# Kernel optimization log

Measured on AMD Instinct MI355X. Metric: run time of the kernel, lower is better.

The kernel has to match this reference:

```python
import jax, jax.numpy as jnp
import numpy as np

B, S, H, NH, NL = 8, 768, 768, 12, 5
HD = H // NH


def setup_inputs() -> dict:
    key = jax.random.key(0)
    ks = jax.random.split(key, 14)
    lim = 1.0 / np.sqrt(H)
    u = lambda k, shape: jax.random.uniform(k, shape, jnp.float32, -lim, lim)
    inp = {}
    inp["hidden_states"] = jax.random.normal(ks[0], (B, S, H), jnp.float32)
    inp["language_ids"] = jax.random.randint(ks[1], (B,), 0, NL)
    inp["attention_mask"] = jnp.ones((B, S), jnp.int32)
    # per-language query/key Linear weights (torch Linear: y = x @ W.T + b)
    inp["Wq_lang"] = u(ks[2], (NL, H, H))
    inp["bq_lang"] = u(ks[3], (NL, H))
    inp["Wk_lang"] = u(ks[4], (NL, H, H))
    inp["bk_lang"] = u(ks[5], (NL, H))
    # nn.MultiheadAttention params
    inp["in_proj_w"] = u(ks[6], (3 * H, H))
    inp["in_proj_b"] = u(ks[7], (3 * H,))
    inp["out_proj_w"] = u(ks[8], (H, H))
    inp["out_proj_b"] = u(ks[9], (H,))
    # alignment matrices: initialized as eye in torch; perturb so products are non-trivial
    inp["align"] = jnp.eye(H, dtype=jnp.float32) + 0.02 * jax.random.normal(ks[10], (NL, NL, H, H), jnp.float32)
    # output projection + layer norm
    inp["proj_w"] = u(ks[11], (H, H))
    inp["proj_b"] = u(ks[12], (H,))
    inp["ln_g"] = jnp.ones((H,), jnp.float32)
    inp["ln_b"] = jnp.zeros((H,), jnp.float32)
    return inp


def reference(hidden_states, language_ids, attention_mask, Wq_lang, bq_lang, Wk_lang, bk_lang,
              in_proj_w, in_proj_b, out_proj_w, out_proj_b, align, proj_w, proj_b, ln_g, ln_b):
    b, s, h = hidden_states.shape
    lang = language_ids
    # language-routed query/key transforms (grouped GEMM via gather of per-lang weights)
    q = jnp.einsum('bsi,boi->bso', hidden_states, Wq_lang[lang]) + bq_lang[lang][:, None, :]
    k = jnp.einsum('bsi,boi->bso', hidden_states, Wk_lang[lang]) + bk_lang[lang][:, None, :]
    # nn.MultiheadAttention (eval mode, no dropout). Note: the torch module's
    # key_padding_mask is always all-False due to a masked_fill(-inf).bool() bug,
    # so no masking is applied -- reproduced faithfully here.
    wq, wk, wv = jnp.split(in_proj_w, 3, axis=0)
    bq_, bk_, bv_ = jnp.split(in_proj_b, 3)
    Q = (jnp.einsum('bsi,oi->bso', q, wq) + bq_).reshape(b, s, NH, HD)
    K = (jnp.einsum('bsi,oi->bso', k, wk) + bk_).reshape(b, s, NH, HD)
    V = (jnp.einsum('bsi,oi->bso', hidden_states, wv) + bv_).reshape(b, s, NH, HD)
    scores = jnp.einsum('bqhd,bkhd->bhqk', Q, K) / np.sqrt(HD).astype(np.float32)
    attn = jax.nn.softmax(scores, axis=-1)  # [b, nh, s, s]
    ctx = jnp.einsum('bhqk,bkhd->bqhd', attn, V).reshape(b, s, h)
    aligned = jnp.einsum('bsi,oi->bso', ctx, out_proj_w) + out_proj_b
    # pairwise alignment chain: for each i, aligned_i @ prod_{j: lang_j != lang_i} A[lang_i, lang_j]
    # (i==j skipped; same-language pairs skipped since no A exists)
    same = lang[:, None] == lang[None, :]  # [b, b]; diagonal is True -> identity
    sel = align[lang[:, None], lang[None, :]]  # [b, b, h, h]
    I = jnp.eye(h, dtype=hidden_states.dtype)
    Smat = jnp.where(same[:, :, None, None], I, sel)  # [b(i), b(j), h, h]
    def step(carry, Sj):  # carry [b,h,h], Sj [b,h,h] for one j across all i
        return carry @ Sj, None
    M, _ = jax.lax.scan(step, jnp.tile(I, (b, 1, 1)), jnp.swapaxes(Smat, 0, 1))
    aligned = jnp.einsum('bsh,bhk->bsk', aligned, M)
    # output projection + residual layer norm
    out = jnp.einsum('bsi,oi->bso', aligned, proj_w) + proj_b
    x = out + hidden_states
    mu = x.mean(-1, keepdims=True)
    var = x.var(-1, keepdims=True)
    return (x - mu) / jnp.sqrt(var + 1e-5) * ln_g + ln_b
```

## Files before the change

kernel.cpp:

```cpp
#include <hip/hip_runtime.h>

#define Bn 8
#define Sn 768
#define Hn 768
#define NHn 12
#define HDn 64
#define NLn 5

typedef unsigned short u16;
typedef __bf16 bf16x8 __attribute__((ext_vector_type(8)));
typedef short s16x8 __attribute__((ext_vector_type(8)));
typedef float f32x4 __attribute__((ext_vector_type(4)));
typedef unsigned short u16x4 __attribute__((ext_vector_type(4)));

static __device__ __forceinline__ float bf2f(u16 v) {
    return __uint_as_float(((unsigned)v) << 16);
}
static __device__ __forceinline__ u16 f2bf(float f) {
    unsigned u = __float_as_uint(f);
    unsigned r = u + 0x7fffu + ((u >> 16) & 1u);
    return (u16)(r >> 16);
}
static __device__ __forceinline__ bf16x8 ld8(const u16* p) {
    return *reinterpret_cast<const bf16x8*>(p);
}
static __device__ __forceinline__ void glds16(const u16* g, u16* l) {
    __builtin_amdgcn_global_load_lds(
        (const __attribute__((address_space(1))) void*)g,
        (__attribute__((address_space(3))) void*)l, 16, 0, 0);
}

#define PREP_NF2B 6912
#define PREP_NTR  1584
__global__ __launch_bounds__(256) void k_prep(
    const float* __restrict__ hidden, u16* __restrict__ hb,
    const float* __restrict__ ipw, u16* __restrict__ ipwb,
    const float* __restrict__ projw, u16* __restrict__ pjwb,
    const float* __restrict__ Wq, const float* __restrict__ Wk,
    const float* __restrict__ opw, u16* __restrict__ S, u16* __restrict__ opwT,
    const float* __restrict__ ipb,
    const float* __restrict__ bq_lang, const float* __restrict__ bk_lang,
    float* __restrict__ beff)
{
    __shared__ float T[64][65];
    const size_t HH = (size_t)Hn * Hn;
    const int bid = blockIdx.x, tid = threadIdx.x;
    if (bid < PREP_NF2B) {
        const int n0 = (int)(Bn * Sn * Hn / 4), n1 = (int)(3 * HH / 4), n2 = (int)(HH / 4);
        int i = bid * 256 + tid;
        const float* s; u16* d; int off;
        if (i < n0)                { s = hidden; d = hb;   off = i; }
        else if (i < n0 + n1)      { s = ipw;    d = ipwb; off = i - n0; }
        else if (i < n0 + n1 + n2) { s = projw;  d = pjwb; off = i - n0 - n1; }
        else return;
        float4 v = reinterpret_cast<const float4*>(s)[off];
        u16x4 o;
        o[0] = f2bf(v.x); o[1] = f2bf(v.y); o[2] = f2bf(v.z); o[3] = f2bf(v.w);
        reinterpret_cast<u16x4*>(d)[off] = o;
    } else if (bid < PREP_NF2B + PREP_NTR) {
        int b2 = bid - PREP_NF2B;
        int z = b2 / 144, r = b2 % 144;
        int bx = r % 12, by = r / 12;
        const float* src;
        u16* dst;
        if (z < 5)       { src = Wq + (size_t)z * HH;       dst = S + (size_t)z * HH; }
        else if (z < 10) { src = Wk + (size_t)(z - 5) * HH; dst = S + (size_t)z * HH; }
        else             { src = opw;                        dst = opwT; }
        int i0 = bx * 64, o0 = by * 64;
        int x = tid & 63, ys = tid >> 6;
        for (int rr = ys; rr < 64; rr += 4)
            T[rr][x] = src[(size_t)(o0 + rr) * Hn + i0 + x];
        __syncthreads();
        for (int rr = ys; rr < 64; rr += 4)
            dst[(size_t)(i0 + rr) * Hn + o0 + x] = f2bf(T[x][rr]);
    } else {
        int b3 = bid - PREP_NF2B - PREP_NTR;
        int ox = b3 % 3, y = b3 / 3;
        int o = ox * 256 + tid;
        int which = y / 5, l = y % 5;
        const float4* w = reinterpret_cast<const float4*>(ipw + (size_t)which * HH + (size_t)o * Hn);
        const float4* bv = reinterpret_cast<const float4*>(((which ? bk_lang : bq_lang) + (size_t)l * Hn));
        float s = 0.f;
        for (int j = 0; j < Hn / 4; ++j) {
            float4 a = w[j], b = bv[j];
            s += a.x * b.x + a.y * b.y + a.z * b.z + a.w * b.w;
        }
        s += ipb[which * Hn + o];
        beff[(size_t)(which * 5 + l) * Hn + o] = s;
    }
}

__global__ __launch_bounds__(256) void k_f2b1(
    const float* __restrict__ s, u16* __restrict__ d, int n)
{
    int i = blockIdx.x * 256 + threadIdx.x;
    if (i >= n) return;
    float4 v = reinterpret_cast<const float4*>(s)[i];
    u16x4 o;
    o[0] = f2bf(v.x); o[1] = f2bf(v.y); o[2] = f2bf(v.z); o[3] = f2bf(v.w);
    reinterpret_cast<u16x4*>(d)[i] = o;
}

__device__ __forceinline__ void gemm128(
    const u16* __restrict__ A, int lda,
    const u16* __restrict__ Bw, int ldb,
    const float* __restrict__ bias,
    const float* __restrict__ addres,
    u16* __restrict__ outH, float* __restrict__ outF,
    u16* __restrict__ outVT, int ldc,
    int K, int m0, int n0, float scale)
{
    __shared__ u16 As[2][128 * 32];
    __shared__ u16 Bs[2][128 * 32];
    const int tid = threadIdx.x;
    const int lane = tid & 63, wave = tid >> 6;
    const int lrow = lane & 15, lquad = lane >> 4;
    const int wm = (wave >> 1) * 64, wn = (wave & 1) * 64;

    const int s0 = tid, s1 = tid + 256;
    const u16* gA0 = A + (size_t)(m0 + (s0 >> 2)) * lda + (s0 & 3) * 8;
    const u16* gA1 = A + (size_t)(m0 + (s1 >> 2)) * lda + (s1 & 3) * 8;
    const u16* gB0 = Bw + (size_t)(n0 + (s0 >> 2)) * ldb + (s0 & 3) * 8;
    const u16* gB1 = Bw + (size_t)(n0 + (s1 >> 2)) * ldb + (s1 & 3) * 8;

    f32x4 z = {0.f, 0.f, 0.f, 0.f};
    f32x4 acc[4][4];
    #pragma unroll
    for (int i = 0; i < 4; ++i)
        #pragma unroll
        for (int j = 0; j < 4; ++j) acc[i][j] = z;

    const int NT = K >> 5;
    auto stage = [&](int buf, int k0) {
        glds16(gA0 + k0, &As[buf][s0 * 8]);
        glds16(gA1 + k0, &As[buf][s1 * 8]);
        glds16(gB0 + k0, &Bs[buf][s0 * 8]);
        glds16(gB1 + k0, &Bs[buf][s1 * 8]);
    };
    auto compute = [&](int buf) {
        bf16x8 af[4], bf_[4];
        #pragma unroll
        for (int i = 0; i < 4; ++i)
            af[i] = ld8(&As[buf][(wm + i * 16 + lrow) * 32 + lquad * 8]);
        #pragma unroll
        for (int j = 0; j < 4; ++j)
            bf_[j] = ld8(&Bs[buf][(wn + j * 16 + lrow) * 32 + lquad * 8]);
        #pragma unroll
        for (int i = 0; i < 4; ++i)
            #pragma unroll
            for (int j = 0; j < 4; ++j)
                acc[i][j] = __builtin_amdgcn_mfma_f32_16x16x32_bf16(af[i], bf_[j], acc[i][j], 0, 0, 0);
    };

    stage(0, 0);
    __syncthreads();
    for (int kt = 1; kt < NT; ++kt) {
        stage(kt & 1, kt * 32);
        compute((kt - 1) & 1);
        __syncthreads();
    }
    compute((NT - 1) & 1);

    #pragma unroll
    for (int i = 0; i < 4; ++i) {
        #pragma unroll
        for (int j = 0; j < 4; ++j) {
            int col = n0 + wn + j * 16 + lrow;
            float bv = bias ? bias[col] : 0.f;
            if (outVT) {
                int row0 = m0 + wm + i * 16 + lquad * 4;
                int bb = row0 / Sn, s = row0 % Sn;
                int hh = col >> 6, dd = col & 63;
                u16x4 o;
                #pragma unroll
                for (int r = 0; r < 4; ++r) o[r] = f2bf((acc[i][j][r] + bv) * scale);
                *reinterpret_cast<u16x4*>(
                    outVT + (((size_t)bb * NHn + hh) * 64 + dd) * Sn + s) = o;
            } else {
                #pragma unroll
                for (int r = 0; r < 4; ++r) {
                    int row = m0 + wm + i * 16 + lquad * 4 + r;
                    float v = (acc[i][j][r] + bv) * scale;
                    if (addres) v += addres[(size_t)row * ldc + col];
                    if (outF) outF[(size_t)row * ldc + col] = v;
                    else      outH[(size_t)row * ldc + col] = f2bf(v);
                }
            }
        }
    }
}

__device__ __forceinline__ void gemm64(
    const u16* __restrict__ A, const u16* __restrict__ Bw,
    u16* __restrict__ outH, int K, int m0, int n0)
{
    __shared__ u16 As[2][64 * 32];
    __shared__ u16 Bs[2][64 * 32];
    const int tid = threadIdx.x;
    const int lane = tid & 63, wave = tid >> 6;
    const int lrow = lane & 15, lquad = lane >> 4;
    const int wm = (wave >> 1) * 32, wn = (wave & 1) * 32;

    const int row = tid >> 2, seg = tid & 3;
    const u16* gA = A + (size_t)(m0 + row) * Hn + seg * 8;
    const u16* gB = Bw + (size_t)(n0 + row) * Hn + seg * 8;

    f32x4 z = {0.f, 0.f, 0.f, 0.f};
    f32x4 acc[2][2];
    #pragma unroll
    for (int i = 0; i < 2; ++i)
        #pragma unroll
        for (int j = 0; j < 2; ++j) acc[i][j] = z;

    const int NT = K >> 5;
    auto stage = [&](int buf, int k0) {
        glds16(gA + k0, &As[buf][tid * 8]);
        glds16(gB + k0, &Bs[buf][tid * 8]);
    };
    auto compute = [&](int buf) {
        bf16x8 af[2], bf_[2];
        #pragma unroll
        for (int i = 0; i < 2; ++i)
            af[i] = ld8(&As[buf][(wm + i * 16 + lrow) * 32 + lquad * 8]);
        #pragma unroll
        for (int j = 0; j < 2; ++j)
            bf_[j] = ld8(&Bs[buf][(wn + j * 16 + lrow) * 32 + lquad * 8]);
        #pragma unroll
        for (int i = 0; i < 2; ++i)
            #pragma unroll
            for (int j = 0; j < 2; ++j)
                acc[i][j] = __builtin_amdgcn_mfma_f32_16x16x32_bf16(af[i], bf_[j], acc[i][j], 0, 0, 0);
    };

    stage(0, 0);
    __syncthreads();
    for (int kt = 1; kt < NT; ++kt) {
        stage(kt & 1, kt * 32);
        compute((kt - 1) & 1);
        __syncthreads();
    }
    compute((NT - 1) & 1);

    #pragma unroll
    for (int i = 0; i < 2; ++i)
        #pragma unroll
        for (int j = 0; j < 2; ++j) {
            int col = n0 + wn + j * 16 + lrow;
            #pragma unroll
            for (int r = 0; r < 4; ++r) {
                int row_ = m0 + wm + i * 16 + lquad * 4 + r;
                outH[(size_t)row_ * Hn + col] = f2bf(acc[i][j][r]);
            }
        }
}


__global__ __launch_bounds__(256) void k_gemm_qkv(
    const u16* __restrict__ A,
    const u16* __restrict__ Sq, const u16* __restrict__ Sk,
    const u16* __restrict__ Wv,
    const float* __restrict__ beff, const float* __restrict__ ipb,
    const int* __restrict__ lang,
    u16* __restrict__ outQ, u16* __restrict__ outK, u16* __restrict__ outVT)
{
    const size_t HH = (size_t)Hn * Hn;
    int z = blockIdx.z;
    int m0 = blockIdx.x * 128, n0 = blockIdx.y * 128;
    int l = lang[blockIdx.x / 6];
    if (z == 0) {
        gemm128(A, Hn, Sq + (size_t)l * HH, Hn, beff + (size_t)l * Hn,
                nullptr, outQ, nullptr, nullptr, Hn, Hn, m0, n0, 0.125f);
    } else if (z == 1) {
        gemm128(A, Hn, Sk + (size_t)l * HH, Hn, beff + (size_t)(5 + l) * Hn,
                nullptr, outK, nullptr, nullptr, Hn, Hn, m0, n0, 1.f);
    } else {
        gemm128(A, Hn, Wv, Hn, ipb + 2 * Hn,
                nullptr, nullptr, nullptr, outVT, Hn, Hn, m0, n0, 1.f);
    }
}

__global__ __launch_bounds__(256) void k_comb10(
    const u16* __restrict__ ipwb, u16* __restrict__ S)
{
    const size_t HH = (size_t)Hn * Hn;
    int z = blockIdx.z;
    const u16* Aop = ipwb + (z < 5 ? 0 : HH);
    gemm128(Aop, Hn, S + (size_t)z * HH, Hn, nullptr, nullptr,
            S + (size_t)(10 + z) * HH, nullptr, nullptr, Hn, Hn,
            blockIdx.x * 128, blockIdx.y * 128, 1.f);
}

__global__ __launch_bounds__(256) void k_chain_first(
    const u16* __restrict__ alignb, const int* __restrict__ lang,
    u16* __restrict__ out5)
{
    const size_t HH = (size_t)Hn * Hn;
    int l = blockIdx.z, lj = lang[Bn - 1];
    u16* dst = out5 + (size_t)l * HH;
    int i0 = blockIdx.x * 64, o0 = blockIdx.y * 64;
    const int tid = threadIdx.x;
    if (lj == l) {
        #pragma unroll
        for (int it = 0; it < 2; ++it) {
            int s = tid + 256 * it;
            int ri = s >> 3, c8 = s & 7;
            s16x8 v;
            #pragma unroll
            for (int e = 0; e < 8; ++e)
                v[e] = (short)((i0 + ri == o0 + c8 * 8 + e) ? 0x3F80 : 0);
            *reinterpret_cast<s16x8*>(dst + (size_t)(i0 + ri) * Hn + o0 + c8 * 8) = v;
        }
    } else {
        const u16* src = alignb + ((size_t)l * NLn + lj) * HH;
        __shared__ u16 T[64][72];
        #pragma unroll
        for (int it = 0; it < 2; ++it) {
            int s = tid + 256 * it;
            int r = s >> 3, c8 = s & 7;
            s16x8 v = *reinterpret_cast<const s16x8*>(
                src + (size_t)(o0 + r) * Hn + i0 + c8 * 8);
            #pragma unroll
            for (int e = 0; e < 8; ++e) T[c8 * 8 + e][r] = (u16)v[e];
        }
        __syncthreads();
        #pragma unroll
        for (int it = 0; it < 2; ++it) {
            int s = tid + 256 * it;
            int ri = s >> 3, c8 = s & 7;
            s16x8 v = *reinterpret_cast<const s16x8*>(&T[ri][c8 * 8]);
            *reinterpret_cast<s16x8*>(dst + (size_t)(i0 + ri) * Hn + o0 + c8 * 8) = v;
        }
    }
}

__global__ __launch_bounds__(256) void k_chain64(
    const u16* __restrict__ Pin, u16* __restrict__ Pout,
    const u16* __restrict__ alignb, const int* __restrict__ lang, int j)
{
    const size_t HH = (size_t)Hn * Hn;
    int l = blockIdx.z;
    int lj = lang[j];
    const u16* Pl = Pin + (size_t)l * HH;
    u16* Po = Pout + (size_t)l * HH;
    int m0 = blockIdx.x * 64, n0 = blockIdx.y * 64;
    if (lj == l) {
        int tid = threadIdx.x;
        #pragma unroll
        for (int it = 0; it < 2; ++it) {
            int s = tid + 256 * it;
            int row = s >> 3, seg = s & 7;
            *reinterpret_cast<s16x8*>(Po + (size_t)(m0 + row) * Hn + n0 + seg * 8) =
                *reinterpret_cast<const s16x8*>(Pl + (size_t)(m0 + row) * Hn + n0 + seg * 8);
        }
    } else {
        const u16* F = alignb + ((size_t)l * NLn + lj) * HH;
        gemm64(Pl, F, Po, Hn, m0, n0);
    }
}

__global__ __launch_bounds__(256) void k_uop(
    const u16* __restrict__ opwT, const u16* __restrict__ MT5,
    const float* __restrict__ opb,
    u16* __restrict__ U5, float* __restrict__ opbeff)
{
    const size_t HH = (size_t)Hn * Hn;
    int bid = blockIdx.x;
    if (bid < 720) {
        int z = bid / 144, r = bid % 144;
        gemm64(opwT, MT5 + (size_t)z * HH, U5 + (size_t)z * HH, Hn,
               (r % 12) * 64, (r / 12) * 64);
    } else {
        int b2 = bid - 720;
        int n = (b2 % 3) * 256 + threadIdx.x;
        int l = b2 / 3;
        const u16* mt = MT5 + ((size_t)l * Hn + n) * Hn;
        float s = 0.f;
        for (int k = 0; k < Hn; k += 8) {
            s16x8 v = *reinterpret_cast<const s16x8*>(mt + k);
            #pragma unroll
            for (int j = 0; j < 8; ++j) s += opb[k + j] * bf2f((u16)v[j]);
        }
        opbeff[(size_t)l * Hn + n] = s;
    }
}

__global__ __launch_bounds__(256) void k_wb2(
    const u16* __restrict__ pjwb, const u16* __restrict__ U5,
    const float* __restrict__ opbeff, const float* __restrict__ projw,
    const float* __restrict__ projb,
    u16* __restrict__ W5, float* __restrict__ bias2)
{
    const size_t HH = (size_t)Hn * Hn;
    int bid = blockIdx.x;
    if (bid < 720) {
        int z = bid / 144, r = bid % 144;
        gemm64(pjwb, U5 + (size_t)z * HH, W5 + (size_t)z * HH, Hn,
               (r % 12) * 64, (r / 12) * 64);
    } else {
        int b2 = bid - 720;
        int m = (b2 % 3) * 256 + threadIdx.x;
        int l = b2 / 3;
        const float4* w = reinterpret_cast<const float4*>(projw + (size_t)m * Hn);
        const float4* ob = reinterpret_cast<const float4*>(opbeff + (size_t)l * Hn);
        float s = 0.f;
        for (int j = 0; j < Hn / 4; ++j) {
            float4 a = w[j], b = ob[j];
            s += a.x * b.x + a.y * b.y + a.z * b.z + a.w * b.w;
        }
        bias2[(size_t)l * Hn + m] = s + projb[m];
    }
}

__global__ __launch_bounds__(256) void k_xfused(
    const u16* __restrict__ ctx, const u16* __restrict__ W5,
    const float* __restrict__ bias2, const int* __restrict__ lang,
    const float* __restrict__ hidden, float* __restrict__ x)
{
    int l = lang[blockIdx.x / 6];
    gemm128(ctx, Hn, W5 + (size_t)l * Hn * Hn, Hn, bias2 + (size_t)l * Hn,
            hidden, nullptr, x, nullptr, Hn, Hn,
            blockIdx.x * 128, blockIdx.y * 128, 1.f);
}

__global__ __launch_bounds__(512) void k_attn(
    const u16* __restrict__ Q, const u16* __restrict__ K,
    const u16* __restrict__ VT, u16* __restrict__ ctx)
{
    __shared__ u16 Ks[2][64 * 64];
    __shared__ u16 Vs[64 * 64];
    __shared__ u16 Pw[8][16 * 72];

    const int bz = blockIdx.z, h = blockIdx.y, q0 = blockIdx.x * 128;
    const int tid = threadIdx.x;
    const int wave = tid >> 6, lane = tid & 63;
    const int lrow = lane & 15, lquad = lane >> 4;
    const int sw = lrow & 7;

    const u16* Qp = Q + ((size_t)(bz * Sn + q0 + wave * 16 + lrow)) * Hn + h * HDn;
    const u16* Kb = K + (size_t)bz * Sn * Hn + h * HDn;
    const u16* Vb = VT + ((size_t)(bz * NHn + h) * 64) * Sn;

    bf16x8 qa0 = ld8(Qp + lquad * 8);
    bf16x8 qa1 = ld8(Qp + 32 + lquad * 8);

    f32x4 z4 = {0.f, 0.f, 0.f, 0.f};
    float m_r[4], l_l[4];
    f32x4 oacc[4];
    #pragma unroll
    for (int r = 0; r < 4; ++r) { m_r[r] = -1e30f; l_l[r] = 0.f; }
    #pragma unroll
    for (int jd = 0; jd < 4; ++jd) oacc[jd] = z4;

    const int vd0 = tid >> 3, vp0 = (tid & 7) ^ (vd0 & 7);
    const u16* vg0 = Vb + (size_t)vd0 * Sn + vp0 * 8;
    s16x8 vr0;

    auto vload = [&](int t0) {
        vr0 = *reinterpret_cast<const s16x8*>(vg0 + t0);
    };
    auto vstore = [&]() {
        *reinterpret_cast<s16x8*>(&Vs[tid * 8]) = vr0;
    };
    auto stageK = [&](int t0, int buf) {
        int row = tid >> 3, p = tid & 7;
        glds16(Kb + (size_t)(t0 + row) * Hn + (p ^ (row & 7)) * 8,
               &Ks[buf][tid * 8]);
    };

    auto compute = [&](int buf) {
        f32x4 sc[4];
        __builtin_amdgcn_s_setprio(1);
        #pragma unroll
        for (int j = 0; j < 4; ++j) {
            int base = (j * 16 + lrow) * 64 + ((lquad ^ sw) * 8);
            f32x4 s = __builtin_amdgcn_mfma_f32_16x16x32_bf16(qa0, ld8(&Ks[buf][base]), z4, 0, 0, 0);
            sc[j] = __builtin_amdgcn_mfma_f32_16x16x32_bf16(qa1, ld8(&Ks[buf][base ^ 32]), s, 0, 0, 0);
        }
        __builtin_amdgcn_s_setprio(0);
        float tmax[4];
        #pragma unroll
        for (int r = 0; r < 4; ++r)
            tmax[r] = fmaxf(fmaxf(sc[0][r], sc[1][r]), fmaxf(sc[2][r], sc[3][r]));
        #pragma unroll
        for (int off = 1; off < 16; off <<= 1)
            #pragma unroll
            for (int r = 0; r < 4; ++r)
                tmax[r] = fmaxf(tmax[r], __shfl_xor(tmax[r], off));
        bool grow = (tmax[0] > m_r[0]) | (tmax[1] > m_r[1]) |
                    (tmax[2] > m_r[2]) | (tmax[3] > m_r[3]);
        if (grow) {
            #pragma unroll
            for (int r = 0; r < 4; ++r) {
                float mn = fmaxf(m_r[r], tmax[r]);
                float a = __expf(m_r[r] - mn);
                m_r[r] = mn;
                l_l[r] *= a;
                #pragma unroll
                for (int jd = 0; jd < 4; ++jd) oacc[jd][r] *= a;
            }
        }
        float ps[4] = {0.f, 0.f, 0.f, 0.f};
        #pragma unroll
        for (int j = 0; j < 4; ++j)
            #pragma unroll
            for (int r = 0; r < 4; ++r) {
                float p = __expf(sc[j][r] - m_r[r]);
                ps[r] += p;
                Pw[wave][(lquad * 4 + r) * 72 + j * 16 + lrow] = f2bf(p);
            }
        #pragma unroll
        for (int r = 0; r < 4; ++r) l_l[r] += ps[r];
        bf16x8 pa0 = ld8(&Pw[wave][lrow * 72 + lquad * 8]);
        bf16x8 pa1 = ld8(&Pw[wave][lrow * 72 + 32 + lquad * 8]);
        __builtin_amdgcn_s_setprio(1);
        #pragma unroll
        for (int jd = 0; jd < 4; ++jd) {
            int vbase = (jd * 16 + lrow) * 64 + ((lquad ^ sw) * 8);
            oacc[jd] = __builtin_amdgcn_mfma_f32_16x16x32_bf16(pa0, ld8(&Vs[vbase]), oacc[jd], 0, 0, 0);
            oacc[jd] = __builtin_amdgcn_mfma_f32_16x16x32_bf16(pa1, ld8(&Vs[vbase ^ 32]), oacc[jd], 0, 0, 0);
        }
        __builtin_amdgcn_s_setprio(0);
    };

    stageK(0, 0);
    vload(0);
    vstore();
    __syncthreads();
    for (int kt = 0; kt < 12; ++kt) {
        if (kt < 11) {
            vload((kt + 1) * 64);
            stageK((kt + 1) * 64, (kt + 1) & 1);
        }
        compute(kt & 1);
        if (kt < 11) {
            __syncthreads();
            vstore();
            __syncthreads();
        }
    }

    #pragma unroll
    for (int off = 1; off < 16; off <<= 1)
        #pragma unroll
        for (int r = 0; r < 4; ++r)
            l_l[r] += __shfl_xor(l_l[r], off);

    float rl[4];
    #pragma unroll
    for (int r = 0; r < 4; ++r) rl[r] = 1.f / l_l[r];
    #pragma unroll
    for (int jd = 0; jd < 4; ++jd)
        #pragma unroll
        for (int r = 0; r < 4; ++r) {
            size_t row = (size_t)bz * Sn + q0 + wave * 16 + lquad * 4 + r;
            ctx[row * Hn + h * HDn + jd * 16 + lrow] = f2bf(oacc[jd][r] * rl[r]);
        }
}

__global__ __launch_bounds__(64) void k_ln(
    float* x, const float* __restrict__ g, const float* __restrict__ beta)
{
    size_t row = blockIdx.x;
    float* xr = x + row * Hn;
    int lane = threadIdx.x;
    float v[12];
    float s = 0.f, ss = 0.f;
    #pragma unroll
    for (int i = 0; i < 12; ++i) {
        v[i] = xr[lane + i * 64];
        s += v[i];
        ss += v[i] * v[i];
    }
    #pragma unroll
    for (int off = 1; off < 64; off <<= 1) {
        s  += __shfl_xor(s, off);
        ss += __shfl_xor(ss, off);
    }
    float mu = s * (1.f / Hn);
    float var = ss * (1.f / Hn) - mu * mu;
    float inv = rsqrtf(var + 1e-5f);
    #pragma unroll
    for (int i = 0; i < 12; ++i) {
        int c = lane + i * 64;
        xr[c] = (v[i] - mu) * inv * g[c] + beta[c];
    }
}

extern "C" void kernel_launch(void* const* d_in, const int* in_sizes, int n_in,
                              void* d_out, int out_size, void* d_ws, size_t ws_size,
                              hipStream_t stream)
{
    (void)in_sizes; (void)n_in; (void)out_size; (void)ws_size;

    const float* hidden  = (const float*)d_in[0];
    const int*   lang    = (const int*)d_in[1];
    const float* Wq_lang = (const float*)d_in[3];
    const float* bq_lang = (const float*)d_in[4];
    const float* Wk_lang = (const float*)d_in[5];
    const float* bk_lang = (const float*)d_in[6];
    const float* ipw     = (const float*)d_in[7];
    const float* ipb     = (const float*)d_in[8];
    const float* opw     = (const float*)d_in[9];
    const float* opb     = (const float*)d_in[10];
    const float* align   = (const float*)d_in[11];
    const float* projw   = (const float*)d_in[12];
    const float* projb   = (const float*)d_in[13];
    const float* ln_g    = (const float*)d_in[14];
    const float* ln_b    = (const float*)d_in[15];
    float* out = (float*)d_out;

    const size_t HH  = (size_t)Hn * Hn;
    const size_t BSH = (size_t)Bn * Sn * Hn;
    const size_t AHH = (size_t)NLn * NLn * HH;

    u16* rA = (u16*)d_ws;
    u16* rB = rA + BSH;
    u16* rC = rB + BSH;
    u16* rD = rC + BSH;
    u16* ipwb = rD + BSH;
    u16* pjwb = ipwb + 3 * HH;
    u16* opwT = pjwb + HH;
    u16* alignb = opwT + HH;
    float* beff   = (float*)(alignb + AHH);
    float* opbeff = beff + 10 * Hn;
    float* bias2  = opbeff + 5 * Hn;

    u16* S = alignb;

    k_prep<<<(unsigned)(PREP_NF2B + PREP_NTR + 30), 256, 0, stream>>>(
        hidden, rA, ipw, ipwb, projw, pjwb,
        Wq_lang, Wk_lang, opw, S, opwT,
        ipb, bq_lang, bk_lang, beff);

    k_comb10<<<dim3(6, 6, 10), 256, 0, stream>>>(ipwb, S);

    k_gemm_qkv<<<dim3(48, 6, 3), 256, 0, stream>>>(
        rA, S + 10 * HH, S + 15 * HH, ipwb + 2 * HH, beff, ipb, lang, rB, rC, rD);

    k_f2b1<<<(unsigned)(AHH / 4 / 256), 256, 0, stream>>>(align, alignb, (int)(AHH / 4));

    k_attn<<<dim3(6, NHn, Bn), 512, 0, stream>>>(rB, rC, rD, rA);

    k_chain_first<<<dim3(12, 12, NLn), 256, 0, stream>>>(alignb, lang, rC);
    u16* Pin = rC;
    u16* Pout = rD;
    for (int j = Bn - 2; j >= 0; --j) {
        k_chain64<<<dim3(12, 12, NLn), 256, 0, stream>>>(Pin, Pout, alignb, lang, j);
        u16* t = Pin; Pin = Pout; Pout = t;
    }

    k_uop<<<735, 256, 0, stream>>>(opwT, Pin, opb, rB, opbeff);
    k_wb2<<<735, 256, 0, stream>>>(pjwb, rB, opbeff, projw, projb, rC, bias2);

    k_xfused<<<dim3(48, 6), 256, 0, stream>>>(rA, rC, bias2, lang, hidden, out);
    k_ln<<<(unsigned)(Bn * Sn), 64, 0, stream>>>(out, ln_g, ln_b);
}
```

Measured before the change: 538.2 us.

## Triple-buffer GEMM LDS pipeline with vmcnt waits and 256-row QKV tiles

Replaces the double-buffered GEMM main loops with a three-stage LDS ring. Each loop waits with explicit s_waitcnt vmcnt plus a raw s_barrier, so two tiles are in flight while one is computed. The QKV projection kernel switches to 256x128 tiles with launch_bounds(256,2) and half as many blocks along M. K is now hardcoded to 768 (24 steps), and the larger LDS footprint and register count could limit occupancy.

```diff
diff --git a/kernel.cpp b/kernel.cpp
--- a/kernel.cpp
+++ b/kernel.cpp
@@ -101,68 +101,84 @@
     reinterpret_cast<u16x4*>(d)[i] = o;
 }
 
-__device__ __forceinline__ void gemm128(
+template<int TM>
+__device__ __forceinline__ void gemm_core(
     const u16* __restrict__ A, int lda,
     const u16* __restrict__ Bw, int ldb,
     const float* __restrict__ bias,
     const float* __restrict__ addres,
     u16* __restrict__ outH, float* __restrict__ outF,
     u16* __restrict__ outVT, int ldc,
-    int K, int m0, int n0, float scale)
-{
-    __shared__ u16 As[2][128 * 32];
-    __shared__ u16 Bs[2][128 * 32];
+    int m0, int n0, float scale)
+{
+    constexpr int MI = TM / 32;
+    constexpr int AIT = TM / 64;
+    __shared__ u16 As[3 * TM * 32];
+    __shared__ u16 Bs[3 * 128 * 32];
     const int tid = threadIdx.x;
     const int lane = tid & 63, wave = tid >> 6;
     const int lrow = lane & 15, lquad = lane >> 4;
-    const int wm = (wave >> 1) * 64, wn = (wave & 1) * 64;
-
-    const int s0 = tid, s1 = tid + 256;
-    const u16* gA0 = A + (size_t)(m0 + (s0 >> 2)) * lda + (s0 & 3) * 8;
-    const u16* gA1 = A + (size_t)(m0 + (s1 >> 2)) * lda + (s1 & 3) * 8;
-    const u16* gB0 = Bw + (size_t)(n0 + (s0 >> 2)) * ldb + (s0 & 3) * 8;
-    const u16* gB1 = Bw + (size_t)(n0 + (s1 >> 2)) * ldb + (s1 & 3) * 8;
+    const int wm = (wave >> 1) * (TM / 2), wn = (wave & 1) * 64;
+
+    const u16* gA = A + (size_t)(m0 + (tid >> 2)) * lda + (tid & 3) * 8;
+    const u16* gB = Bw + (size_t)(n0 + (tid >> 2)) * ldb + (tid & 3) * 8;
 
     f32x4 z = {0.f, 0.f, 0.f, 0.f};
-    f32x4 acc[4][4];
-    #pragma unroll
-    for (int i = 0; i < 4; ++i)
+    f32x4 acc[MI][4];
+    #pragma unroll
+    for (int i = 0; i < MI; ++i)
         #pragma unroll
         for (int j = 0; j < 4; ++j) acc[i][j] = z;
 
-    const int NT = K >> 5;
-    auto stage = [&](int buf, int k0) {
-        glds16(gA0 + k0, &As[buf][s0 * 8]);
-        glds16(gA1 + k0, &As[buf][s1 * 8]);
-        glds16(gB0 + k0, &Bs[buf][s0 * 8]);
-        glds16(gB1 + k0, &Bs[buf][s1 * 8]);
-    };
-    auto compute = [&](int buf) {
-        bf16x8 af[4], bf_[4];
-        #pragma unroll
-        for (int i = 0; i < 4; ++i)
-            af[i] = ld8(&As[buf][(wm + i * 16 + lrow) * 32 + lquad * 8]);
+    auto stage = [&](int bs, int k0) {
+        #pragma unroll
+        for (int it = 0; it < AIT; ++it)
+            glds16(gA + (size_t)(it * 64) * lda + k0, &As[bs * TM * 32 + (tid + 256 * it) * 8]);
+        #pragma unroll
+        for (int it = 0; it < 2; ++it)
+            glds16(gB + (size_t)(it * 64) * ldb + k0, &Bs[bs * 128 * 32 + (tid + 256 * it) * 8]);
+    };
+    auto compute = [&](int bc) {
+        const u16* Ab = &As[bc * TM * 32];
+        const u16* Bb = &Bs[bc * 128 * 32];
+        bf16x8 af[MI], bf_[4];
+        #pragma unroll
+        for (int i = 0; i < MI; ++i)
+            af[i] = ld8(&Ab[(wm + i * 16 + lrow) * 32 + lquad * 8]);
         #pragma unroll
         for (int j = 0; j < 4; ++j)
-            bf_[j] = ld8(&Bs[buf][(wn + j * 16 + lrow) * 32 + lquad * 8]);
-        #pragma unroll
-        for (int i = 0; i < 4; ++i)
+            bf_[j] = ld8(&Bb[(wn + j * 16 + lrow) * 32 + lquad * 8]);
+        #pragma unroll
+        for (int i = 0; i < MI; ++i)
             #pragma unroll
             for (int j = 0; j < 4; ++j)
                 acc[i][j] = __builtin_amdgcn_mfma_f32_16x16x32_bf16(af[i], bf_[j], acc[i][j], 0, 0, 0);
     };
 
     stage(0, 0);
-    __syncthreads();
-    for (int kt = 1; kt < NT; ++kt) {
-        stage(kt & 1, kt * 32);
-        compute((kt - 1) & 1);
-        __syncthreads();
-    }
-    compute((NT - 1) & 1);
-
-    #pragma unroll
-    for (int i = 0; i < 4; ++i) {
+    stage(1, 32);
+    int bc = 0, bs = 2;
+    for (int kt = 0; kt < 24; ++kt) {
+        if (kt < 23) {
+            if constexpr (TM == 256) {
+                asm volatile("s_waitcnt vmcnt(6)" ::: "memory");
+            } else {
+                asm volatile("s_waitcnt vmcnt(4)" ::: "memory");
+            }
+        } else {
+            asm volatile("s_waitcnt vmcnt(0)" ::: "memory");
+        }
+        __builtin_amdgcn_s_barrier();
+        if (kt < 22) {
+            stage(bs, (kt + 2) * 32);
+            bs = (bs == 2) ? 0 : bs + 1;
+        }
+        compute(bc);
+        bc = (bc == 2) ? 0 : bc + 1;
+    }
+
+    #pragma unroll
+    for (int i = 0; i < MI; ++i) {
         #pragma unroll
         for (int j = 0; j < 4; ++j) {
             int col = n0 + wn + j * 16 + lrow;
@@ -192,18 +208,17 @@
 
 __device__ __forceinline__ void gemm64(
     const u16* __restrict__ A, const u16* __restrict__ Bw,
-    u16* __restrict__ outH, int K, int m0, int n0)
-{
-    __shared__ u16 As[2][64 * 32];
-    __shared__ u16 Bs[2][64 * 32];
+    u16* __restrict__ outH, int m0, int n0)
+{
+    __shared__ u16 As[3 * 64 * 32];
+    __shared__ u16 Bs[3 * 64 * 32];
     const int tid = threadIdx.x;
     const int lane = tid & 63, wave = tid >> 6;
     const int lrow = lane & 15, lquad = lane >> 4;
     const int wm = (wave >> 1) * 32, wn = (wave & 1) * 32;
 
-    const int row = tid >> 2, seg = tid & 3;
-    const u16* gA = A + (size_t)(m0 + row) * Hn + seg * 8;
-    const u16* gB = Bw + (size_t)(n0 + row) * Hn + seg * 8;
+    const u16* gA = A + (size_t)(m0 + (tid >> 2)) * Hn + (tid & 3) * 8;
+    const u16* gB = Bw + (size_t)(n0 + (tid >> 2)) * Hn + (tid & 3) * 8;
 
     f32x4 z = {0.f, 0.f, 0.f, 0.f};
     f32x4 acc[2][2];
@@ -212,19 +227,20 @@
         #pragma unroll
         for (int j = 0; j < 2; ++j) acc[i][j] = z;
 
-    const int NT = K >> 5;
-    auto stage = [&](int buf, int k0) {
-        glds16(gA + k0, &As[buf][tid * 8]);
-        glds16(gB + k0, &Bs[buf][tid * 8]);
-    };
-    auto compute = [&](int buf) {
+    auto stage = [&](int bs, int k0) {
+        glds16(gA + k0, &As[bs * 64 * 32 + tid * 8]);
+        glds16(gB + k0, &Bs[bs * 64 * 32 + tid * 8]);
+    };
+    auto compute = [&](int bc) {
+        const u16* Ab = &As[bc * 64 * 32];
+        const u16* Bb = &Bs[bc * 64 * 32];
         bf16x8 af[2], bf_[2];
         #pragma unroll
         for (int i = 0; i < 2; ++i)
-            af[i] = ld8(&As[buf][(wm + i * 16 + lrow) * 32 + lquad * 8]);
+            af[i] = ld8(&Ab[(wm + i * 16 + lrow) * 32 + lquad * 8]);
         #pragma unroll
         for (int j = 0; j < 2; ++j)
-            bf_[j] = ld8(&Bs[buf][(wn + j * 16 + lrow) * 32 + lquad * 8]);
+            bf_[j] = ld8(&Bb[(wn + j * 16 + lrow) * 32 + lquad * 8]);
         #pragma unroll
         for (int i = 0; i < 2; ++i)
             #pragma unroll
@@ -233,13 +249,22 @@
     };
 
     stage(0, 0);
-    __syncthreads();
-    for (int kt = 1; kt < NT; ++kt) {
-        stage(kt & 1, kt * 32);
-        compute((kt - 1) & 1);
-        __syncthreads();
-    }
-    compute((NT - 1) & 1);
+    stage(1, 32);
+    int bc = 0, bs = 2;
+    for (int kt = 0; kt < 24; ++kt) {
+        if (kt < 23) {
+            asm volatile("s_waitcnt vmcnt(2)" ::: "memory");
+        } else {
+            asm volatile("s_waitcnt vmcnt(0)" ::: "memory");
+        }
+        __builtin_amdgcn_s_barrier();
+        if (kt < 22) {
+            stage(bs, (kt + 2) * 32);
+            bs = (bs == 2) ? 0 : bs + 1;
+        }
+        compute(bc);
+        bc = (bc == 2) ? 0 : bc + 1;
+    }
 
     #pragma unroll
     for (int i = 0; i < 2; ++i)
@@ -255,7 +280,7 @@
 }
 
 
-__global__ __launch_bounds__(256) void k_gemm_qkv(
+__global__ __launch_bounds__(256, 2) void k_gemm_qkv(
     const u16* __restrict__ A,
     const u16* __restrict__ Sq, const u16* __restrict__ Sk,
     const u16* __restrict__ Wv,
@@ -265,17 +290,17 @@
 {
     const size_t HH = (size_t)Hn * Hn;
     int z = blockIdx.z;
-    int m0 = blockIdx.x * 128, n0 = blockIdx.y * 128;
-    int l = lang[blockIdx.x / 6];
+    int m0 = blockIdx.x * 256, n0 = blockIdx.y * 128;
+    int l = lang[blockIdx.x / 3];
     if (z == 0) {
-        gemm128(A, Hn, Sq + (size_t)l * HH, Hn, beff + (size_t)l * Hn,
-                nullptr, outQ, nullptr, nullptr, Hn, Hn, m0, n0, 0.125f);
+        gemm_core<256>(A, Hn, Sq + (size_t)l * HH, Hn, beff + (size_t)l * Hn,
+                       nullptr, outQ, nullptr, nullptr, Hn, m0, n0, 0.125f);
     } else if (z == 1) {
-        gemm128(A, Hn, Sk + (size_t)l * HH, Hn, beff + (size_t)(5 + l) * Hn,
-                nullptr, outK, nullptr, nullptr, Hn, Hn, m0, n0, 1.f);
+        gemm_core<256>(A, Hn, Sk + (size_t)l * HH, Hn, beff + (size_t)(5 + l) * Hn,
+                       nullptr, outK, nullptr, nullptr, Hn, m0, n0, 1.f);
     } else {
-        gemm128(A, Hn, Wv, Hn, ipb + 2 * Hn,
-                nullptr, nullptr, nullptr, outVT, Hn, Hn, m0, n0, 1.f);
+        gemm_core<256>(A, Hn, Wv, Hn, ipb + 2 * Hn,
+                       nullptr, nullptr, nullptr, outVT, Hn, m0, n0, 1.f);
     }
 }
 
@@ -285,9 +310,9 @@
     const size_t HH = (size_t)Hn * Hn;
     int z = blockIdx.z;
     const u16* Aop = ipwb + (z < 5 ? 0 : HH);
-    gemm128(Aop, Hn, S + (size_t)z * HH, Hn, nullptr, nullptr,
-            S + (size_t)(10 + z) * HH, nullptr, nullptr, Hn, Hn,
-            blockIdx.x * 128, blockIdx.y * 128, 1.f);
+    gemm_core<128>(Aop, Hn, S + (size_t)z * HH, Hn, nullptr, nullptr,
+                   S + (size_t)(10 + z) * HH, nullptr, nullptr, Hn,
+                   blockIdx.x * 128, blockIdx.y * 128, 1.f);
 }
 
 __global__ __launch_bounds__(256) void k_chain_first(
@@ -354,7 +379,7 @@
         }
     } else {
         const u16* F = alignb + ((size_t)l * NLn + lj) * HH;
-        gemm64(Pl, F, Po, Hn, m0, n0);
+        gemm64(Pl, F, Po, m0, n0);
     }
 }
 
@@ -367,7 +392,7 @@
     int bid = blockIdx.x;
     if (bid < 720) {
         int z = bid / 144, r = bid % 144;
-        gemm64(opwT, MT5 + (size_t)z * HH, U5 + (size_t)z * HH, Hn,
+        gemm64(opwT, MT5 + (size_t)z * HH, U5 + (size_t)z * HH,
                (r % 12) * 64, (r / 12) * 64);
     } else {
         int b2 = bid - 720;
@@ -394,7 +419,7 @@
     int bid = blockIdx.x;
     if (bid < 720) {
         int z = bid / 144, r = bid % 144;
-        gemm64(pjwb, U5 + (size_t)z * HH, W5 + (size_t)z * HH, Hn,
+        gemm64(pjwb, U5 + (size_t)z * HH, W5 + (size_t)z * HH,
                (r % 12) * 64, (r / 12) * 64);
     } else {
         int b2 = bid - 720;
@@ -417,9 +442,9 @@
     const float* __restrict__ hidden, float* __restrict__ x)
 {
     int l = lang[blockIdx.x / 6];
-    gemm128(ctx, Hn, W5 + (size_t)l * Hn * Hn, Hn, bias2 + (size_t)l * Hn,
-            hidden, nullptr, x, nullptr, Hn, Hn,
-            blockIdx.x * 128, blockIdx.y * 128, 1.f);
+    gemm_core<128>(ctx, Hn, W5 + (size_t)l * Hn * Hn, Hn, bias2 + (size_t)l * Hn,
+                   hidden, nullptr, x, nullptr, Hn,
+                   blockIdx.x * 128, blockIdx.y * 128, 1.f);
 }
 
 __global__ __launch_bounds__(512) void k_attn(
@@ -634,7 +659,7 @@
 
     k_comb10<<<dim3(6, 6, 10), 256, 0, stream>>>(ipwb, S);
 
-    k_gemm_qkv<<<dim3(48, 6, 3), 256, 0, stream>>>(
+    k_gemm_qkv<<<dim3(24, 6, 3), 256, 0, stream>>>(
         rA, S + 10 * HH, S + 15 * HH, ipwb + 2 * HH, beff, ipb, lang, rB, rC, rD);
 
     k_f2b1<<<(unsigned)(AHH / 4 / 256), 256, 0, stream>>>(align, alignb, (int)(AHH / 4));
```

New measurement: 513.9 us. 1.05x faster.
